# Performance work log

Measured on AMD Instinct MI355X. Metric: run time of the kernel, lower is better.

## Reference

```python
import jax, jax.numpy as jnp
import numpy as np

N = 192      # num_tracklets
D = 4096     # feature dim (hardcoded in original forward via expand(..., 4096))


def setup_inputs() -> dict:
    key = jax.random.key(0)
    ks = jax.random.split(key, 8)
    s = 0.02
    f   = jax.random.normal(ks[0], (N, D), jnp.float32)
    # learned parameters (torch Linear convention: W [out, in], y = x @ W.T + b)
    Wc1 = jax.random.normal(ks[1], (D, D),    jnp.float32) * s
    bc1 = jnp.zeros((D,), jnp.float32)
    W1  = jax.random.normal(ks[2], (2048, D), jnp.float32) * s
    b1  = jnp.zeros((2048,), jnp.float32)
    W2  = jax.random.normal(ks[3], (1024, 2048), jnp.float32) * s
    b2  = jnp.zeros((1024,), jnp.float32)
    W3  = jax.random.normal(ks[4], (512, 1024), jnp.float32) * s
    b3  = jnp.zeros((512,), jnp.float32)
    Ws  = jax.random.normal(ks[5], (1, 512), jnp.float32) * s
    bs  = jnp.zeros((1,), jnp.float32)
    return {"f": f, "Wc1": Wc1, "bc1": bc1, "W1": W1, "b1": b1,
            "W2": W2, "b2": b2, "W3": W3, "b3": b3, "Ws": Ws, "bs": bs}


def reference(f, Wc1, bc1, W1, b1, W2, b2, W3, b3, Ws, bs):
    # camera-feature removal: f <- f - relu(cam_fc1(f))
    cam = jax.nn.relu(f @ Wc1.T + bc1)            # [N, D]
    g = f - cam                                   # [N, D]
    # pairwise broadcast abs-diff: [N, N, D]
    dist = jnp.abs(g[:, None, :] - g[None, :, :])
    # 3-layer MLP affinity head + sigmoid
    h = jax.nn.relu(jnp.einsum('ijd,kd->ijk', dist, W1) + b1)   # [N, N, 2048]
    h = jax.nn.relu(h @ W2.T + b2)                              # [N, N, 1024]
    h = jax.nn.relu(h @ W3.T + b3)                              # [N, N, 512]
    A = jax.nn.sigmoid(h @ Ws.T + bs)[..., 0]                   # [N, N]
    return A
```

## Files before the change

### kernel.cpp

```cpp
#include <hip/hip_runtime.h>
#include <hip/hip_bf16.h>


typedef unsigned short u16;
typedef __attribute__((ext_vector_type(8))) short    bf16x8;
typedef __attribute__((ext_vector_type(8))) unsigned short u16x8;
typedef __attribute__((ext_vector_type(4))) float    f32x4;

#define MFMA16(a, b, c) __builtin_amdgcn_mfma_f32_16x16x32_bf16((a), (b), (c), 0, 0, 0)

#define NTRK 192
#define TRI  18528
#define TRIP 18688

__device__ __forceinline__ unsigned int pkbf(float lo, float hi) {
    __hip_bfloat162 h2 = __float22bfloat162_rn(make_float2(lo, hi));
    return *reinterpret_cast<unsigned int*>(&h2);
}
__device__ __forceinline__ void gll16(void* lds_uniform, const void* gsrc) {
    __builtin_amdgcn_global_load_lds(
        (__attribute__((address_space(1))) void*)(gsrc),
        (__attribute__((address_space(3))) void*)(lds_uniform),
        16, 0, 0);
}
__device__ __forceinline__ void tri_decode(int r, int& oi, int& oj) {
    double a = 192.5;
    int i = (int)(a - sqrt(a * a - 2.0 * (double)r));
    i = i < 0 ? 0 : (i > 191 ? 191 : i);
    while (i < 191 && (i + 1) * (385 - (i + 1)) / 2 <= r) ++i;
    while (i > 0 && i * (385 - i) / 2 > r) --i;
    int j = i + (r - i * (385 - i) / 2);
    oi = i; oj = j > 191 ? 191 : j;
}

#define CVT_N 7143424
__global__ __launch_bounds__(256)
void k_cvt_all(const float* __restrict__ s0, u16* __restrict__ d0,
               const float* __restrict__ s1, u16* __restrict__ d1,
               const float* __restrict__ s2, u16* __restrict__ d2,
               const float* __restrict__ s3, u16* __restrict__ d3,
               const float* __restrict__ s4, u16* __restrict__ d4)
{
    int i = blockIdx.x * 256 + threadIdx.x;
    if (i >= CVT_N) return;
    const float* s; u16* d; int j;
    if      (i < 4194304) { s = s0; d = d0; j = i; }
    else if (i < 6291456) { s = s1; d = d1; j = i - 4194304; }
    else if (i < 6815744) { s = s2; d = d2; j = i - 6291456; }
    else if (i < 6946816) { s = s3; d = d3; j = i - 6815744; }
    else                  { s = s4; d = d4; j = i - 6946816; }
    f32x4 v = ((const f32x4*)s)[j];
    ((uint2*)d)[j] = make_uint2(pkbf(v.x, v.y), pkbf(v.z, v.w));
}

__global__ __launch_bounds__(256, 2)
void k_cam(const u16* __restrict__ fb, const u16* __restrict__ Wc1b,
           float* __restrict__ camp)
{
    __shared__ __align__(16) u16 As[64 * 64];
    __shared__ __align__(16) u16 Bs[128 * 64];
    const int t = threadIdx.x, l = t & 63, w = t >> 6;
    const int m0 = blockIdx.x * 64, n0 = blockIdx.y * 128;
    const int kbeg = blockIdx.z * 1024, kend = kbeg + 1024;
    const int lr8 = l >> 3;
    const int lc8 = (l & 7) ^ lr8;
    const u16* Ab = fb   + (size_t)(m0 + w * 16 + lr8) * 4096 + lc8 * 8;
    const u16* Bb = Wc1b + (size_t)(n0 + w * 32 + lr8) * 4096 + lc8 * 8;
    f32x4 acc[2][4] = {};
    const int wr = (w >> 1) * 32, wc = (w & 1) * 64;
    const int lrow = l & 15, lq = l >> 4, s = lrow & 7;

    for (int k0 = kbeg; k0 < kend; k0 += 64) {
        __syncthreads();
#pragma unroll
        for (int q = 0; q < 2; ++q)
            gll16(&As[(w * 16 + q * 8) * 64], Ab + (size_t)q * 8 * 4096 + k0);
#pragma unroll
        for (int q = 0; q < 4; ++q)
            gll16(&Bs[(w * 32 + q * 8) * 64], Bb + (size_t)q * 8 * 4096 + k0);
        __syncthreads();
#pragma unroll
        for (int kk8 = 0; kk8 < 8; kk8 += 4) {
            const int co = ((kk8 + lq) ^ s) * 8;
            bf16x8 af[2], bfr[4];
#pragma unroll
            for (int mi = 0; mi < 2; ++mi)
                af[mi] = *(const bf16x8*)&As[(wr + mi * 16 + lrow) * 64 + co];
#pragma unroll
            for (int ni = 0; ni < 4; ++ni)
                bfr[ni] = *(const bf16x8*)&Bs[(wc + ni * 16 + lrow) * 64 + co];
#pragma unroll
            for (int mi = 0; mi < 2; ++mi)
#pragma unroll
                for (int ni = 0; ni < 4; ++ni)
                    acc[mi][ni] = MFMA16(af[mi], bfr[ni], acc[mi][ni]);
        }
    }
    float* cz = camp + (size_t)blockIdx.z * 192 * 4096;
    const int rq = (l >> 4) * 4;
#pragma unroll
    for (int ni = 0; ni < 4; ++ni) {
        const int col = n0 + wc + ni * 16 + lrow;
#pragma unroll
        for (int mi = 0; mi < 2; ++mi) {
            const int rbase = m0 + wr + mi * 16 + rq;
#pragma unroll
            for (int v = 0; v < 4; ++v)
                cz[(size_t)(rbase + v) * 4096 + col] = acc[mi][ni][v];
        }
    }
}

__global__ __launch_bounds__(256)
void k_gfin(const float* __restrict__ camp, const float* __restrict__ bc1,
            const float* __restrict__ f, float* __restrict__ g)
{
    const int i = blockIdx.x * 256 + threadIdx.x;
    const int col4 = (i * 4) & 4095;
    f32x4 p0 = ((const f32x4*)camp)[i];
    f32x4 p1 = ((const f32x4*)(camp + 786432))[i];
    f32x4 p2 = ((const f32x4*)(camp + 1572864))[i];
    f32x4 p3 = ((const f32x4*)(camp + 2359296))[i];
    f32x4 b = *(const f32x4*)(bc1 + col4);
    f32x4 fv = ((const f32x4*)f)[i];
    f32x4 r;
    r.x = fv.x - fmaxf(p0.x + p1.x + p2.x + p3.x + b.x, 0.0f);
    r.y = fv.y - fmaxf(p0.y + p1.y + p2.y + p3.y + b.y, 0.0f);
    r.z = fv.z - fmaxf(p0.z + p1.z + p2.z + p3.z + b.z, 0.0f);
    r.w = fv.w - fmaxf(p0.w + p1.w + p2.w + p3.w + b.w, 0.0f);
    ((f32x4*)g)[i] = r;
}

__global__ __launch_bounds__(256)
void k_distgen(const float* __restrict__ g, u16* __restrict__ dist, int row0)
{
    const int r = blockIdx.y;
    const int c = blockIdx.x * 256 + threadIdx.x;
    int pi, pj; tri_decode(row0 + r, pi, pj);
    const float* gi = g + (size_t)pi * 4096 + c * 8;
    const float* gj = g + (size_t)pj * 4096 + c * 8;
    f32x4 a0 = ((const f32x4*)gi)[0], a1 = ((const f32x4*)gi)[1];
    f32x4 b0 = ((const f32x4*)gj)[0], b1 = ((const f32x4*)gj)[1];
    uint4 o;
    o.x = pkbf(fabsf(b0.x - a0.x), fabsf(b0.y - a0.y));
    o.y = pkbf(fabsf(b0.z - a0.z), fabsf(b0.w - a0.w));
    o.z = pkbf(fabsf(b1.x - a1.x), fabsf(b1.y - a1.y));
    o.w = pkbf(fabsf(b1.z - a1.z), fabsf(b1.w - a1.w));
    *reinterpret_cast<uint4*>(dist + (size_t)r * 4096 + c * 8) = o;
}

__global__ __launch_bounds__(256, 2)
void k_gemm_relu(const u16* __restrict__ A, const u16* __restrict__ B,
                 const float* __restrict__ bias, u16* __restrict__ C,
                 int N, int K)
{
    __shared__ __align__(16) u16 As[128 * 64];
    __shared__ __align__(16) u16 Bs[128 * 64];
    const int t = threadIdx.x, l = t & 63, w = t >> 6;
    const int m0 = blockIdx.y * 128, n0 = blockIdx.x * 128;
    const int lr8 = l >> 3;
    const int lc8 = (l & 7) ^ lr8;
    const u16* Ab = A + (size_t)(m0 + w * 32 + lr8) * K + lc8 * 8;
    const u16* Bb = B + (size_t)(n0 + w * 32 + lr8) * K + lc8 * 8;
    f32x4 acc[4][4] = {};
    const int wr = (w >> 1) * 64, wc = (w & 1) * 64;
    const int lrow = l & 15, lq = l >> 4, s = lrow & 7;

    for (int k0 = 0; k0 < K; k0 += 64) {
        __syncthreads();
#pragma unroll
        for (int q = 0; q < 4; ++q) {
            gll16(&As[(w * 32 + q * 8) * 64], Ab + (size_t)q * 8 * K + k0);
            gll16(&Bs[(w * 32 + q * 8) * 64], Bb + (size_t)q * 8 * K + k0);
        }
        __syncthreads();
#pragma unroll
        for (int kk8 = 0; kk8 < 8; kk8 += 4) {
            const int co = ((kk8 + lq) ^ s) * 8;
            bf16x8 af[4], bfr[4];
#pragma unroll
            for (int mi = 0; mi < 4; ++mi)
                af[mi] = *(const bf16x8*)&As[(wr + mi * 16 + lrow) * 64 + co];
#pragma unroll
            for (int ni = 0; ni < 4; ++ni)
                bfr[ni] = *(const bf16x8*)&Bs[(wc + ni * 16 + lrow) * 64 + co];
#pragma unroll
            for (int mi = 0; mi < 4; ++mi)
#pragma unroll
                for (int ni = 0; ni < 4; ++ni)
                    acc[mi][ni] = MFMA16(af[mi], bfr[ni], acc[mi][ni]);
        }
    }
    const int rq = (l >> 4) * 4;
#pragma unroll
    for (int ni = 0; ni < 4; ++ni) {
        const int col = n0 + wc + ni * 16 + lrow;
        const float bv = bias[col];
#pragma unroll
        for (int mi = 0; mi < 4; ++mi) {
            const int rbase = m0 + wr + mi * 16 + rq;
#pragma unroll
            for (int v = 0; v < 4; ++v) {
                float x = fmaxf(acc[mi][ni][v] + bv, 0.0f);
                C[(size_t)(rbase + v) * N + col] = (u16)(pkbf(x, 0.0f) & 0xFFFF);
            }
        }
    }
}

__global__ __launch_bounds__(256, 2)
void k_gemm3(const u16* __restrict__ A, const u16* __restrict__ B,
             const float* __restrict__ bias, const float* __restrict__ Wsv,
             float* __restrict__ logit, int r0)
{
    const int N = 512, K = 1024;
    __shared__ __align__(16) u16 As[128 * 64];
    __shared__ __align__(16) u16 Bs[128 * 64];
    const int t = threadIdx.x, l = t & 63, w = t >> 6;
    const int m0 = blockIdx.y * 128, n0 = blockIdx.x * 128;
    const int lr8 = l >> 3;
    const int lc8 = (l & 7) ^ lr8;
    const u16* Ab = A + (size_t)(m0 + w * 32 + lr8) * K + lc8 * 8;
    const u16* Bb = B + (size_t)(n0 + w * 32 + lr8) * K + lc8 * 8;
    f32x4 acc[4][4] = {};
    const int wr = (w >> 1) * 64, wc = (w & 1) * 64;
    const int lrow = l & 15, lq = l >> 4, s = lrow & 7;

    for (int k0 = 0; k0 < K; k0 += 64) {
        __syncthreads();
#pragma unroll
        for (int q = 0; q < 4; ++q) {
            gll16(&As[(w * 32 + q * 8) * 64], Ab + (size_t)q * 8 * K + k0);
            gll16(&Bs[(w * 32 + q * 8) * 64], Bb + (size_t)q * 8 * K + k0);
        }
        __syncthreads();
#pragma unroll
        for (int kk8 = 0; kk8 < 8; kk8 += 4) {
            const int co = ((kk8 + lq) ^ s) * 8;
            bf16x8 af[4], bfr[4];
#pragma unroll
            for (int mi = 0; mi < 4; ++mi)
                af[mi] = *(const bf16x8*)&As[(wr + mi * 16 + lrow) * 64 + co];
#pragma unroll
            for (int ni = 0; ni < 4; ++ni)
                bfr[ni] = *(const bf16x8*)&Bs[(wc + ni * 16 + lrow) * 64 + co];
#pragma unroll
            for (int mi = 0; mi < 4; ++mi)
#pragma unroll
                for (int ni = 0; ni < 4; ++ni)
                    acc[mi][ni] = MFMA16(af[mi], bfr[ni], acc[mi][ni]);
        }
    }
    const int rq = (l >> 4) * 4;
    float wv[4], bv[4];
#pragma unroll
    for (int ni = 0; ni < 4; ++ni) {
        const int col = n0 + wc + ni * 16 + lrow;
        wv[ni] = Wsv[col];
        bv[ni] = bias[col];
    }
#pragma unroll
    for (int mi = 0; mi < 4; ++mi) {
#pragma unroll
        for (int v = 0; v < 4; ++v) {
            float p = 0.0f;
#pragma unroll
            for (int ni = 0; ni < 4; ++ni)
                p += fmaxf(acc[mi][ni][v] + bv[ni], 0.0f) * wv[ni];
            p += __shfl_xor(p, 1, 64);
            p += __shfl_xor(p, 2, 64);
            p += __shfl_xor(p, 4, 64);
            p += __shfl_xor(p, 8, 64);
            if (lrow == 0)
                atomicAdd(&logit[r0 + m0 + wr + mi * 16 + rq + v], p);
        }
    }
}

__global__ __launch_bounds__(256)
void k_sig(const float* __restrict__ logit, const float* __restrict__ bsv,
           float* __restrict__ out)
{
    const int r = blockIdx.x * 256 + threadIdx.x;
    if (r >= TRI) return;
    int pi, pj; tri_decode(r, pi, pj);
    float v = 1.0f / (1.0f + __expf(-(logit[r] + bsv[0])));
    out[pi * NTRK + pj] = v;
    out[pj * NTRK + pi] = v;
}

extern "C" void kernel_launch(void* const* d_in, const int* in_sizes, int n_in,
                              void* d_out, int out_size, void* d_ws, size_t ws_size,
                              hipStream_t stream)
{
    const float* f   = (const float*)d_in[0];
    const float* Wc1 = (const float*)d_in[1];
    const float* bc1 = (const float*)d_in[2];
    const float* W1  = (const float*)d_in[3];
    const float* b1  = (const float*)d_in[4];
    const float* W2  = (const float*)d_in[5];
    const float* b2  = (const float*)d_in[6];
    const float* W3  = (const float*)d_in[7];
    const float* b3  = (const float*)d_in[8];
    const float* Wsv = (const float*)d_in[9];
    const float* bsv = (const float*)d_in[10];
    float* out = (float*)d_out;

    char* wsb = (char*)d_ws;
    size_t off = 0;
    u16*   W1b   = (u16*)(wsb + off);  off += (size_t)2048 * 4096 * 2;
    u16*   W2b   = (u16*)(wsb + off);  off += (size_t)1024 * 2048 * 2;
    u16*   W3b   = (u16*)(wsb + off);  off += (size_t)512  * 1024 * 2;
    u16*   fb    = (u16*)(wsb + off);  off += (size_t)192  * 4096 * 2;
    float* g     = (float*)(wsb + off); off += (size_t)192 * 4096 * 4;
    float* logit = (float*)(wsb + off); off += (size_t)TRIP * 4;
    const size_t chunkbase = off;
    u16*   Wc1b = (u16*)(wsb + chunkbase);
    float* camp = (float*)(wsb + chunkbase + (size_t)4096 * 4096 * 2);
    const size_t phaseA = (size_t)4096 * 4096 * 2 + (size_t)4 * 192 * 4096 * 4;

    const int Rcand[6] = {18688, 14336, 9344, 4736, 2432, 1280};
    int R = 128;
    for (int c = 0; c < 6; ++c) {
        size_t chunk = (size_t)Rcand[c] * 12288;
        if (chunk < phaseA) chunk = phaseA;
        if (chunkbase + chunk <= ws_size) { R = Rcand[c]; break; }
    }
    u16* dist = (u16*)(wsb + chunkbase);
    u16* h1 = dist + (size_t)R * 4096;
    u16* h2 = dist;

    hipMemsetAsync(logit, 0, (size_t)TRIP * 4, stream);
    k_cvt_all<<<(CVT_N + 255) / 256, 256, 0, stream>>>(
        Wc1, Wc1b, W1, W1b, W2, W2b, W3, W3b, f, fb);
    k_cam<<<dim3(3, 32, 4), 256, 0, stream>>>(fb, Wc1b, camp);
    k_gfin<<<768, 256, 0, stream>>>(camp, bc1, f, g);

    for (int r0 = 0; r0 < TRI; r0 += R) {
        int rows = TRIP - r0; if (rows > R) rows = R;
        k_distgen<<<dim3(2, rows), 256, 0, stream>>>(g, dist, r0);
        k_gemm_relu<<<dim3(16, rows / 128), 256, 0, stream>>>(dist, W1b, b1, h1, 2048, 4096);
        k_gemm_relu<<<dim3(8,  rows / 128), 256, 0, stream>>>(h1, W2b, b2, h2, 1024, 2048);
        k_gemm3<<<dim3(4, rows / 128), 256, 0, stream>>>(h2, W3b, b3, Wsv, logit, r0);
    }
    k_sig<<<(TRI + 255) / 256, 256, 0, stream>>>(logit, bsv, out);
}
```

Baseline: 642.6 us.

## Rewrite MLP GEMM as 256x256 tiles with double-buffered phased LDS pipeline

The two big bf16 GEMMs move from 128x128 tiles with 256 threads and a single LDS buffer to 256x256 tiles with 512 threads (8 waves) and double-buffered LDS. K is processed in 128-wide steps split into eight phases that interleave global-to-LDS loads with MFMA work, using explicit vmcnt/lgkmcnt waits, barriers and s_setprio. The aim is to hide load latency and raise arithmetic intensity per block. Chunk sizes are rounded to multiples of 256 rows to match the new tiling. In exchange it needs 128KB of LDS per block and more accumulator registers, and the hand-placed waitcnt and barrier logic is fragile.

```diff
diff --git a/kernel.cpp b/kernel.cpp
--- a/kernel.cpp
+++ b/kernel.cpp
@@ -149,56 +149,100 @@
     *reinterpret_cast<uint4*>(dist + (size_t)r * 4096 + c * 8) = o;
 }
 
-__global__ __launch_bounds__(256, 2)
+__global__ __launch_bounds__(512, 2)
 void k_gemm_relu(const u16* __restrict__ A, const u16* __restrict__ B,
                  const float* __restrict__ bias, u16* __restrict__ C,
                  int N, int K)
 {
-    __shared__ __align__(16) u16 As[128 * 64];
-    __shared__ __align__(16) u16 Bs[128 * 64];
+    __shared__ __align__(16) u16 As[2][256 * 64];
+    __shared__ __align__(16) u16 Bs[2][256 * 64];
     const int t = threadIdx.x, l = t & 63, w = t >> 6;
-    const int m0 = blockIdx.y * 128, n0 = blockIdx.x * 128;
+    const int m0 = blockIdx.y * 256, n0 = blockIdx.x * 256;
     const int lr8 = l >> 3;
     const int lc8 = (l & 7) ^ lr8;
-    const u16* Ab = A + (size_t)(m0 + w * 32 + lr8) * K + lc8 * 8;
-    const u16* Bb = B + (size_t)(n0 + w * 32 + lr8) * K + lc8 * 8;
-    f32x4 acc[4][4] = {};
-    const int wr = (w >> 1) * 64, wc = (w & 1) * 64;
+    const int wm = w >> 2, wn = w & 3;
     const int lrow = l & 15, lq = l >> 4, s = lrow & 7;
 
-    for (int k0 = 0; k0 < K; k0 += 64) {
-        __syncthreads();
-#pragma unroll
-        for (int q = 0; q < 4; ++q) {
-            gll16(&As[(w * 32 + q * 8) * 64], Ab + (size_t)q * 8 * K + k0);
-            gll16(&Bs[(w * 32 + q * 8) * 64], Bb + (size_t)q * 8 * K + k0);
-        }
-        __syncthreads();
-#pragma unroll
-        for (int kk8 = 0; kk8 < 8; kk8 += 4) {
-            const int co = ((kk8 + lq) ^ s) * 8;
-            bf16x8 af[4], bfr[4];
-#pragma unroll
-            for (int mi = 0; mi < 4; ++mi)
-                af[mi] = *(const bf16x8*)&As[(wr + mi * 16 + lrow) * 64 + co];
-#pragma unroll
-            for (int ni = 0; ni < 4; ++ni)
-                bfr[ni] = *(const bf16x8*)&Bs[(wc + ni * 16 + lrow) * 64 + co];
-#pragma unroll
-            for (int mi = 0; mi < 4; ++mi)
-#pragma unroll
-                for (int ni = 0; ni < 4; ++ni)
-                    acc[mi][ni] = MFMA16(af[mi], bfr[ni], acc[mi][ni]);
-        }
-    }
-    const int rq = (l >> 4) * 4;
+    const u16* Ab = A + (size_t)(m0 + w * 8 + lr8) * K + lc8 * 8;
+    const u16* Bb = B + (size_t)(n0 + w * 8 + lr8) * K + lc8 * 8;
+    const size_t row64 = (size_t)64 * K;
+
+    f32x4 acc[8][4] = {};
+    const int NIT = K >> 7;
+
+#define SA(kt_, ha_) do { \
+    u16* lb_ = &As[(kt_) & 1][((ha_) * 128 + w * 8) * 64]; \
+    const u16* gs_ = Ab + (size_t)(ha_) * 128 * K + (kt_) * 64; \
+    gll16(lb_, gs_); gll16(lb_ + 64 * 64, gs_ + row64); \
+} while (0)
+#define SB(kt_, hb_) do { \
+    u16* lb_ = &Bs[(kt_) & 1][((hb_) * 128 + w * 8) * 64]; \
+    const u16* gs_ = Bb + (size_t)(hb_) * 128 * K + (kt_) * 64; \
+    gll16(lb_, gs_); gll16(lb_ + 64 * 64, gs_ + row64); \
+} while (0)
+
+#define PHASE(p_, q_, RDB_, STG_, WAIT_) do { \
+    bf16x8 af[2][2]; \
+    _Pragma("unroll") \
+    for (int kk = 0; kk < 2; ++kk) { \
+        _Pragma("unroll") \
+        for (int mi = 0; mi < 2; ++mi) \
+            af[kk][mi] = *(const bf16x8*)&As[p_][(wm * 128 + (q_) * 32 + mi * 16 + lrow) * 64 + ((kk * 4 + lq) ^ s) * 8]; \
+        if (RDB_) { \
+            _Pragma("unroll") \
+            for (int ni = 0; ni < 4; ++ni) \
+                bf[kk][ni] = *(const bf16x8*)&Bs[p_][(wn * 64 + ni * 16 + lrow) * 64 + ((kk * 4 + lq) ^ s) * 8]; \
+        } \
+    } \
+    STG_ \
+    __builtin_amdgcn_s_barrier(); \
+    asm volatile("s_waitcnt lgkmcnt(0)" ::: "memory"); \
+    __builtin_amdgcn_s_setprio(1); \
+    _Pragma("unroll") \
+    for (int kk = 0; kk < 2; ++kk) \
+        _Pragma("unroll") \
+        for (int mi = 0; mi < 2; ++mi) \
+            _Pragma("unroll") \
+            for (int ni = 0; ni < 4; ++ni) \
+                acc[(q_) * 2 + mi][ni] = MFMA16(af[kk][mi], bf[kk][ni], acc[(q_) * 2 + mi][ni]); \
+    __builtin_amdgcn_s_setprio(0); \
+    WAIT_ \
+    __builtin_amdgcn_s_barrier(); \
+} while (0)
+
+    SA(0, 0); SA(0, 1); SB(0, 0); SB(0, 1);
+    SB(1, 0); SB(1, 1);
+    asm volatile("s_waitcnt vmcnt(4)" ::: "memory");
+    __builtin_amdgcn_s_barrier();
+
+    for (int it = 0; it < NIT; ++it) {
+        const int kt = 2 * it;
+        const bool hn = (it + 1 < NIT);
+        bf16x8 bf[2][4];
+        PHASE(0, 0, 1, SA(kt + 1, 0);, );
+        PHASE(0, 1, 0, SA(kt + 1, 1);, );
+        PHASE(0, 2, 0, if (hn) SB(kt + 2, 0);, );
+        PHASE(0, 3, 0, if (hn) SB(kt + 2, 1);,
+              if (hn) { asm volatile("s_waitcnt vmcnt(4)" ::: "memory"); }
+              else    { asm volatile("s_waitcnt vmcnt(0)" ::: "memory"); } );
+        PHASE(1, 0, 1, if (hn) SA(kt + 2, 0);, );
+        PHASE(1, 1, 0, if (hn) SA(kt + 2, 1);, );
+        PHASE(1, 2, 0, if (hn) SB(kt + 3, 0);, );
+        PHASE(1, 3, 0, if (hn) SB(kt + 3, 1);,
+              if (hn) { asm volatile("s_waitcnt vmcnt(4)" ::: "memory"); } );
+    }
+#undef SA
+#undef SB
+#undef PHASE
+
+    const int rq = lq * 4;
 #pragma unroll
     for (int ni = 0; ni < 4; ++ni) {
-        const int col = n0 + wc + ni * 16 + lrow;
+        const int col = n0 + wn * 64 + ni * 16 + lrow;
         const float bv = bias[col];
 #pragma unroll
-        for (int mi = 0; mi < 4; ++mi) {
-            const int rbase = m0 + wr + mi * 16 + rq;
+        for (int mi = 0; mi < 8; ++mi) {
+            const int rbase = m0 + wm * 128 + mi * 16 + rq;
 #pragma unroll
             for (int v = 0; v < 4; ++v) {
                 float x = fmaxf(acc[mi][ni][v] + bv, 0.0f);
@@ -319,8 +363,8 @@
     float* camp = (float*)(wsb + chunkbase + (size_t)4096 * 4096 * 2);
     const size_t phaseA = (size_t)4096 * 4096 * 2 + (size_t)4 * 192 * 4096 * 4;
 
-    const int Rcand[6] = {18688, 14336, 9344, 4736, 2432, 1280};
-    int R = 128;
+    const int Rcand[6] = {18688, 14336, 9472, 4864, 2560, 1280};
+    int R = 256;
     for (int c = 0; c < 6; ++c) {
         size_t chunk = (size_t)Rcand[c] * 12288;
         if (chunk < phaseA) chunk = phaseA;
@@ -339,8 +383,8 @@
     for (int r0 = 0; r0 < TRI; r0 += R) {
         int rows = TRIP - r0; if (rows > R) rows = R;
         k_distgen<<<dim3(2, rows), 256, 0, stream>>>(g, dist, r0);
-        k_gemm_relu<<<dim3(16, rows / 128), 256, 0, stream>>>(dist, W1b, b1, h1, 2048, 4096);
-        k_gemm_relu<<<dim3(8,  rows / 128), 256, 0, stream>>>(h1, W2b, b2, h2, 1024, 2048);
+        k_gemm_relu<<<dim3(8, rows / 256), 512, 0, stream>>>(dist, W1b, b1, h1, 2048, 4096);
+        k_gemm_relu<<<dim3(4, rows / 256), 512, 0, stream>>>(h1, W2b, b2, h2, 1024, 2048);
         k_gemm3<<<dim3(4, rows / 128), 256, 0, stream>>>(h2, W3b, b3, Wsv, logit, r0);
     }
     k_sig<<<(TRI + 255) / 256, 256, 0, stream>>>(logit, bsv, out);
```

Measured after the change: 771.5 us. 20.1% more time.

## Add 256x256 eight-wave pipelined bf16 GEMM for the first two MLP layers

Applied to the files above, without the earlier changes.

Adds a new GEMM kernel with 256x256 output tiles and 8 waves. It double-buffers A and B tiles in LDS through direct global-to-LDS loads and interleaves sub-tile LDS reads, prefetches and MFMA bursts, with barriers and raised wave priority around the MFMA bursts. The kernel replaces the 128x128 GEMM for the dist→h1 and h1→h2 layers when the chunk row count is a multiple of 256 and at least 8192. The goal is more operand reuse per LDS byte and better overlap of memory traffic with matrix math. The cost is much larger LDS use, which limits occupancy, and a fragile hand-written waitcnt schedule.

```diff
diff --git a/kernel.cpp b/kernel.cpp
--- a/kernel.cpp
+++ b/kernel.cpp
@@ -4,7 +4,6 @@
 
 typedef unsigned short u16;
 typedef __attribute__((ext_vector_type(8))) short    bf16x8;
-typedef __attribute__((ext_vector_type(8))) unsigned short u16x8;
 typedef __attribute__((ext_vector_type(4))) float    f32x4;
 
 #define MFMA16(a, b, c) __builtin_amdgcn_mfma_f32_16x16x32_bf16((a), (b), (c), 0, 0, 0)
@@ -208,6 +207,115 @@
     }
 }
 
+__global__ __launch_bounds__(512, 2)
+void k_gemm8(const u16* __restrict__ A, const u16* __restrict__ B,
+             const float* __restrict__ bias, u16* __restrict__ C,
+             int N, int K)
+{
+    __shared__ __align__(16) u16 As[2][256 * 64];
+    __shared__ __align__(16) u16 Bs[2][256 * 64];
+    const int t = threadIdx.x, l = t & 63, w = t >> 6;
+    const int m0 = blockIdx.y * 256, n0 = blockIdx.x * 256;
+    const int wm = w >> 2, wn = w & 3;
+    const int lrow = l & 15, lq = l >> 4, s8 = lrow & 7;
+    const int lr8 = l >> 3, lc8 = (l & 7) ^ lr8;
+    const int NIT = K >> 6;
+
+    const u16* Asrc = A + (size_t)(m0 + w * 8 + lr8) * K + lc8 * 8;
+    const u16* Bsrc = B + (size_t)(n0 + w * 8 + lr8) * K + lc8 * 8;
+
+    f32x4 acc[8][4] = {};
+    bf16x8 af[4][2], bf[2][2][2];
+
+#define STG(isB_, tile_, half_) do { \
+    const int tt = (tile_) < NIT ? (tile_) : NIT - 1; \
+    u16* dst_ = (isB_) ? &Bs[tt & 1][0] : &As[tt & 1][0]; \
+    const u16* sb_ = ((isB_) ? Bsrc : Asrc) + (size_t)((half_) * 128) * K + (size_t)tt * 64; \
+    gll16(&dst_[((half_) * 128 + w * 8) * 64], sb_); \
+    gll16(&dst_[((half_) * 128 + 64 + w * 8) * 64], sb_ + (size_t)64 * K); \
+} while (0)
+
+#define RDA(r_) do { \
+    _Pragma("unroll") for (int mi = 0; mi < 4; ++mi) { \
+        const int row_ = wm * 128 + (r_) * 64 + mi * 16 + lrow; \
+        _Pragma("unroll") for (int kk = 0; kk < 2; ++kk) \
+            af[mi][kk] = *(const bf16x8*)&Ard[row_ * 64 + ((kk * 4 + lq) ^ s8) * 8]; \
+    } \
+} while (0)
+
+#define RDB(c_) do { \
+    _Pragma("unroll") for (int ni = 0; ni < 2; ++ni) { \
+        const int row_ = wn * 32 + (c_) * 128 + ni * 16 + lrow; \
+        _Pragma("unroll") for (int kk = 0; kk < 2; ++kk) \
+            bf[c_][ni][kk] = *(const bf16x8*)&Brd[row_ * 64 + ((kk * 4 + lq) ^ s8) * 8]; \
+    } \
+} while (0)
+
+#define MM(r_, c_) do { \
+    __builtin_amdgcn_s_setprio(1); \
+    _Pragma("unroll") for (int mi = 0; mi < 4; ++mi) \
+        _Pragma("unroll") for (int ni = 0; ni < 2; ++ni) \
+            _Pragma("unroll") for (int kk = 0; kk < 2; ++kk) \
+                acc[(r_) * 4 + mi][(c_) * 2 + ni] = \
+                    MFMA16(af[mi][kk], bf[c_][ni][kk], acc[(r_) * 4 + mi][(c_) * 2 + ni]); \
+    __builtin_amdgcn_s_setprio(0); \
+} while (0)
+
+#define SBAR asm volatile("s_barrier" ::: "memory")
+
+    STG(0, 0, 0); STG(0, 0, 1); STG(1, 0, 0); STG(1, 0, 1); STG(0, 1, 0);
+    asm volatile("s_waitcnt vmcnt(2)" ::: "memory");
+    SBAR;
+
+    for (int kt = 0; kt < NIT; ++kt) {
+        const u16* Ard = &As[kt & 1][0];
+        const u16* Brd = &Bs[kt & 1][0];
+        RDA(0); RDB(0); STG(0, kt + 1, 1);
+        SBAR;
+        MM(0, 0);
+        asm volatile("s_waitcnt vmcnt(4)" ::: "memory");
+        SBAR;
+        RDB(1); STG(1, kt + 1, 0);
+        SBAR;
+        MM(0, 1);
+        SBAR;
+        RDA(1); STG(1, kt + 1, 1);
+        SBAR;
+        MM(1, 0);
+        SBAR;
+        STG(0, kt + 2, 0);
+        SBAR;
+        MM(1, 1);
+        asm volatile("s_waitcnt vmcnt(4)" ::: "memory");
+        SBAR;
+    }
+    asm volatile("s_waitcnt vmcnt(0)" ::: "memory");
+#undef STG
+#undef RDA
+#undef RDB
+#undef MM
+#undef SBAR
+
+#pragma unroll
+    for (int c = 0; c < 2; ++c)
+#pragma unroll
+        for (int ni = 0; ni < 2; ++ni) {
+            const int col = n0 + wn * 32 + c * 128 + ni * 16 + lrow;
+            const float bv = bias[col];
+#pragma unroll
+            for (int r = 0; r < 2; ++r)
+#pragma unroll
+                for (int mi = 0; mi < 4; ++mi) {
+                    const int rbase = m0 + wm * 128 + r * 64 + mi * 16 + lq * 4;
+#pragma unroll
+                    for (int v = 0; v < 4; ++v) {
+                        float x = fmaxf(acc[r * 4 + mi][c * 2 + ni][v] + bv, 0.0f);
+                        C[(size_t)(rbase + v) * N + col] = (u16)(pkbf(x, 0.0f) & 0xFFFF);
+                    }
+                }
+        }
+}
+
 __global__ __launch_bounds__(256, 2)
 void k_gemm3(const u16* __restrict__ A, const u16* __restrict__ B,
              const float* __restrict__ bias, const float* __restrict__ Wsv,
@@ -339,8 +447,13 @@
     for (int r0 = 0; r0 < TRI; r0 += R) {
         int rows = TRIP - r0; if (rows > R) rows = R;
         k_distgen<<<dim3(2, rows), 256, 0, stream>>>(g, dist, r0);
-        k_gemm_relu<<<dim3(16, rows / 128), 256, 0, stream>>>(dist, W1b, b1, h1, 2048, 4096);
-        k_gemm_relu<<<dim3(8,  rows / 128), 256, 0, stream>>>(h1, W2b, b2, h2, 1024, 2048);
+        if ((rows & 255) == 0 && rows >= 8192) {
+            k_gemm8<<<dim3(8, rows / 256), 512, 0, stream>>>(dist, W1b, b1, h1, 2048, 4096);
+            k_gemm8<<<dim3(4, rows / 256), 512, 0, stream>>>(h1, W2b, b2, h2, 1024, 2048);
+        } else {
+            k_gemm_relu<<<dim3(16, rows / 128), 256, 0, stream>>>(dist, W1b, b1, h1, 2048, 4096);
+            k_gemm_relu<<<dim3(8,  rows / 128), 256, 0, stream>>>(h1, W2b, b2, h2, 1024, 2048);
+        }
         k_gemm3<<<dim3(4, rows / 128), 256, 0, stream>>>(h2, W3b, b3, Wsv, logit, r0);
     }
     k_sig<<<(TRI + 255) / 256, 256, 0, stream>>>(logit, bsv, out);
```

New measurement: 698.2 us. 8.6% more time.
